# Kernel optimization log

Hardware: AMD Instinct MI355X
Metric: run time of the kernel (lower is better)

## Reference

```python
import jax, jax.numpy as jnp
import numpy as np

N_NODES = 100000
N_EDGES = 1600000
D_IN = 256
D_OUT = 64
AVG_DEG = N_EDGES // N_NODES  # 16


def setup_inputs() -> dict:
    key = jax.random.key(0)
    k1, k2, k3 = jax.random.split(key, 3)
    X = jax.random.normal(k1, (N_NODES, D_IN), dtype=jnp.float32)
    weights = jax.random.normal(k2, (D_IN, D_OUT), dtype=jnp.float32) * (1.0 / np.sqrt(D_IN))
    # CSR with uniform degree for a valid structure (load balance is a kernel concern, not math)
    row_pointers = jnp.arange(N_NODES + 1, dtype=jnp.int64) * AVG_DEG
    column_index = jax.random.randint(k3, (N_EDGES,), 0, N_NODES, dtype=jnp.int64)
    # GNNAdvisor precomputes degrees as d^{-1/2} for symmetric GCN normalization
    deg = (row_pointers[1:] - row_pointers[:-1]).astype(jnp.float32)
    degrees = 1.0 / jnp.sqrt(jnp.maximum(deg, 1.0))
    return {"X": X, "weights": weights, "row_pointers": row_pointers,
            "column_index": column_index, "degrees": degrees}


def reference(X, weights, row_pointers, column_index, degrees):
    # Dense transform: [N, D_in] @ [D_in, D_out] -> [N, D_out]
    X_prime = jnp.matmul(X, weights)
    E = column_index.shape[0]
    # CSR row ids for each edge (destination node of the aggregation)
    row_ids = jnp.searchsorted(row_pointers, jnp.arange(E, dtype=row_pointers.dtype), side='right') - 1
    # out[i] = d_i^{-1/2} * sum_{j in N(i)} d_j^{-1/2} * X'[j]
    gathered = X_prime[column_index] * degrees[column_index][:, None]  # [E, D_out]
    agg = jax.ops.segment_sum(gathered, row_ids, num_segments=row_pointers.shape[0] - 1)
    return agg * degrees[:, None]
```

## Files before the change

### kernel.cpp

```cpp
#include <hip/hip_runtime.h>
#include <hip/hip_bf16.h>


constexpr int D_IN  = 256;
constexpr int D_OUT = 64;
constexpr int WT_LD = D_IN + 8;

typedef short  s8v  __attribute__((ext_vector_type(8)));
typedef __bf16 bf8v __attribute__((ext_vector_type(8)));
typedef float  f32x4 __attribute__((ext_vector_type(4)));
typedef unsigned short us8v __attribute__((ext_vector_type(8)));

union BF8 { bf8v b; s8v s; };

__global__ __launch_bounds__(256) void gemm_bf16_kernel(
    const float* __restrict__ X, const float* __restrict__ W,
    const float* __restrict__ deg, unsigned short* __restrict__ Xp, int n)
{
    __shared__ __bf16 Wt[D_OUT][WT_LD];

    const int tid = threadIdx.x;

    #pragma unroll
    for (int i = 0; i < 16; ++i) {
        const int f4 = tid + i * 256;
        const int k  = f4 >> 4;
        const int c4 = (f4 & 15) * 4;
        const float4 w = *reinterpret_cast<const float4*>(&W[(size_t)k * D_OUT + c4]);
        Wt[c4 + 0][k] = (__bf16)w.x;
        Wt[c4 + 1][k] = (__bf16)w.y;
        Wt[c4 + 2][k] = (__bf16)w.z;
        Wt[c4 + 3][k] = (__bf16)w.w;
    }
    __syncthreads();

    const int wid  = tid >> 6;
    const int lane = tid & 63;
    const int lrow = lane & 15;
    const int kgrp = lane >> 4;

    const int row0 = blockIdx.x * 64 + wid * 16;
    if (row0 >= n) return;
    const int grow = row0 + lrow;
    const int xr   = grow < n ? grow : n - 1;

    f32x4 acc[4] = {};

    const float* xrow = X + (size_t)xr * D_IN + kgrp * 8;
    const __bf16* wt0 = &Wt[lrow][kgrp * 8];

    #pragma unroll
    for (int ks = 0; ks < 8; ++ks) {
        const int k0 = ks * 32;
        const float4 x0 = *reinterpret_cast<const float4*>(xrow + k0);
        const float4 x1 = *reinterpret_cast<const float4*>(xrow + k0 + 4);
        BF8 xf;
        xf.b[0] = (__bf16)x0.x; xf.b[1] = (__bf16)x0.y;
        xf.b[2] = (__bf16)x0.z; xf.b[3] = (__bf16)x0.w;
        xf.b[4] = (__bf16)x1.x; xf.b[5] = (__bf16)x1.y;
        xf.b[6] = (__bf16)x1.z; xf.b[7] = (__bf16)x1.w;

        #pragma unroll
        for (int f = 0; f < 4; ++f) {
            const s8v wf = *reinterpret_cast<const s8v*>(wt0 + (size_t)f * 16 * WT_LD + k0);
            acc[f] = __builtin_amdgcn_mfma_f32_16x16x32_bf16(wf, xf.s, acc[f], 0, 0, 0);
        }
    }

    if (grow < n) {
        const float d = deg[grow];
        #pragma unroll
        for (int f = 0; f < 4; ++f) {
            ushort4 v;
            __bf16 b0 = (__bf16)(acc[f][0] * d);
            __bf16 b1 = (__bf16)(acc[f][1] * d);
            __bf16 b2 = (__bf16)(acc[f][2] * d);
            __bf16 b3 = (__bf16)(acc[f][3] * d);
            v.x = *reinterpret_cast<unsigned short*>(&b0);
            v.y = *reinterpret_cast<unsigned short*>(&b1);
            v.z = *reinterpret_cast<unsigned short*>(&b2);
            v.w = *reinterpret_cast<unsigned short*>(&b3);
            *reinterpret_cast<ushort4*>(
                &Xp[(size_t)grow * D_OUT + f * 16 + kgrp * 4]) = v;
        }
    }
}

__global__ __launch_bounds__(256) void agg_kernel(
    const unsigned short* __restrict__ Xp, const int* __restrict__ rp,
    const int* __restrict__ ci, const float* __restrict__ deg,
    float* __restrict__ out, int n)
{
    const int node = blockIdx.x * 32 + (threadIdx.x >> 3);
    if (node >= n) return;
    const int c8 = (threadIdx.x & 7) * 8;

    const int e0 = rp[node];
    const int e1 = rp[node + 1];

    float acc[8] = {};
    int e = e0;
    for (; e + 4 <= e1; e += 4) {
        const int j0 = ci[e + 0];
        const int j1 = ci[e + 1];
        const int j2 = ci[e + 2];
        const int j3 = ci[e + 3];
        const us8v v0 = *reinterpret_cast<const us8v*>(&Xp[(size_t)j0 * D_OUT + c8]);
        const us8v v1 = *reinterpret_cast<const us8v*>(&Xp[(size_t)j1 * D_OUT + c8]);
        const us8v v2 = *reinterpret_cast<const us8v*>(&Xp[(size_t)j2 * D_OUT + c8]);
        const us8v v3 = *reinterpret_cast<const us8v*>(&Xp[(size_t)j3 * D_OUT + c8]);
        #pragma unroll
        for (int j = 0; j < 8; ++j) {
            acc[j] += __uint_as_float((unsigned)v0[j] << 16);
            acc[j] += __uint_as_float((unsigned)v1[j] << 16);
            acc[j] += __uint_as_float((unsigned)v2[j] << 16);
            acc[j] += __uint_as_float((unsigned)v3[j] << 16);
        }
    }
    for (; e < e1; ++e) {
        const us8v v = *reinterpret_cast<const us8v*>(&Xp[(size_t)ci[e] * D_OUT + c8]);
        #pragma unroll
        for (int j = 0; j < 8; ++j)
            acc[j] += __uint_as_float((unsigned)v[j] << 16);
    }

    const float d = deg[node];
    float4 o0 = make_float4(acc[0] * d, acc[1] * d, acc[2] * d, acc[3] * d);
    float4 o1 = make_float4(acc[4] * d, acc[5] * d, acc[6] * d, acc[7] * d);
    float* op = out + (size_t)node * D_OUT + c8;
    *reinterpret_cast<float4*>(op)     = o0;
    *reinterpret_cast<float4*>(op + 4) = o1;
}

extern "C" void kernel_launch(void* const* d_in, const int* in_sizes, int n_in,
                              void* d_out, int out_size, void* d_ws, size_t ws_size,
                              hipStream_t stream)
{
    const float* X   = (const float*)d_in[0];
    const float* W   = (const float*)d_in[1];
    const int*   rp  = (const int*)d_in[2];
    const int*   ci  = (const int*)d_in[3];
    const float* deg = (const float*)d_in[4];
    float* out = (float*)d_out;
    unsigned short* Xp = (unsigned short*)d_ws;

    const int n = in_sizes[4];

    const int gemm_blocks = (n + 63) / 64;
    gemm_bf16_kernel<<<gemm_blocks, 256, 0, stream>>>(X, W, deg, Xp, n);

    const int agg_blocks = (n + 31) / 32;
    agg_kernel<<<agg_blocks, 256, 0, stream>>>(Xp, rp, ci, deg, out, n);
}
```

Measured before the change: 57.32 us.

## Pre-transpose weights once, make GEMM persistent, batch 16 gathers in aggregation

Adds a tiny kernel that converts and transposes W to bf16 in workspace once, so each GEMM block copies it into shared memory with vector loads instead of redoing the scattered transpose. The GEMM becomes a grid-stride persistent kernel with 391 blocks that loop over 16-row tiles, which amortises the weight staging across many tiles. The aggregation adds a fast path for degree-16 aligned rows that loads the indices as int4 and issues all 16 neighbour gathers before accumulating, raising memory-level parallelism at the cost of more registers. It also adds an extra kernel launch, and the fixed grid size may leave some compute units underused.

```diff
diff --git a/kernel.cpp b/kernel.cpp
--- a/kernel.cpp
+++ b/kernel.cpp
@@ -13,24 +13,30 @@
 
 union BF8 { bf8v b; s8v s; };
 
+__global__ void prep_w_kernel(const float* __restrict__ W,
+                              unsigned short* __restrict__ Wt_g)
+{
+    const int c = blockIdx.x;
+    const int k = threadIdx.x;
+    __bf16 b = (__bf16)W[(size_t)k * D_OUT + c];
+    Wt_g[(size_t)c * D_IN + k] = *reinterpret_cast<unsigned short*>(&b);
+}
+
 __global__ __launch_bounds__(256) void gemm_bf16_kernel(
-    const float* __restrict__ X, const float* __restrict__ W,
-    const float* __restrict__ deg, unsigned short* __restrict__ Xp, int n)
+    const float* __restrict__ X, const unsigned short* __restrict__ Wt_g,
+    const float* __restrict__ deg, unsigned short* __restrict__ Xp,
+    int n, int ntiles)
 {
-    __shared__ __bf16 Wt[D_OUT][WT_LD];
+    __shared__ unsigned short Wt[D_OUT][WT_LD];
 
     const int tid = threadIdx.x;
 
-    #pragma unroll
-    for (int i = 0; i < 16; ++i) {
-        const int f4 = tid + i * 256;
-        const int k  = f4 >> 4;
-        const int c4 = (f4 & 15) * 4;
-        const float4 w = *reinterpret_cast<const float4*>(&W[(size_t)k * D_OUT + c4]);
-        Wt[c4 + 0][k] = (__bf16)w.x;
-        Wt[c4 + 1][k] = (__bf16)w.y;
-        Wt[c4 + 2][k] = (__bf16)w.z;
-        Wt[c4 + 3][k] = (__bf16)w.w;
+    {
+        const int c = tid >> 2, seg = tid & 3;
+        const us8v* src = reinterpret_cast<const us8v*>(Wt_g + (size_t)c * D_IN + seg * 64);
+        us8v* dst = reinterpret_cast<us8v*>(&Wt[c][seg * 64]);
+        #pragma unroll
+        for (int i = 0; i < 8; ++i) dst[i] = src[i];
     }
     __syncthreads();
 
@@ -39,49 +45,50 @@
     const int lrow = lane & 15;
     const int kgrp = lane >> 4;
 
-    const int row0 = blockIdx.x * 64 + wid * 16;
-    if (row0 >= n) return;
-    const int grow = row0 + lrow;
-    const int xr   = grow < n ? grow : n - 1;
+    const unsigned short* wt0 = &Wt[lrow][kgrp * 8];
+    const int wstride = gridDim.x << 2;
 
-    f32x4 acc[4] = {};
+    for (int tile = blockIdx.x * 4 + wid; tile < ntiles; tile += wstride) {
+        const int grow = tile * 16 + lrow;
+        const int xr   = grow < n ? grow : n - 1;
+        const float* xrow = X + (size_t)xr * D_IN + kgrp * 8;
 
-    const float* xrow = X + (size_t)xr * D_IN + kgrp * 8;
-    const __bf16* wt0 = &Wt[lrow][kgrp * 8];
-
-    #pragma unroll
-    for (int ks = 0; ks < 8; ++ks) {
-        const int k0 = ks * 32;
-        const float4 x0 = *reinterpret_cast<const float4*>(xrow + k0);
-        const float4 x1 = *reinterpret_cast<const float4*>(xrow + k0 + 4);
-        BF8 xf;
-        xf.b[0] = (__bf16)x0.x; xf.b[1] = (__bf16)x0.y;
-        xf.b[2] = (__bf16)x0.z; xf.b[3] = (__bf16)x0.w;
-        xf.b[4] = (__bf16)x1.x; xf.b[5] = (__bf16)x1.y;
-        xf.b[6] = (__bf16)x1.z; xf.b[7] = (__bf16)x1.w;
+        f32x4 acc[4] = {};
 
         #pragma unroll
-        for (int f = 0; f < 4; ++f) {
-            const s8v wf = *reinterpret_cast<const s8v*>(wt0 + (size_t)f * 16 * WT_LD + k0);
-            acc[f] = __builtin_amdgcn_mfma_f32_16x16x32_bf16(wf, xf.s, acc[f], 0, 0, 0);
+        for (int ks = 0; ks < 8; ++ks) {
+            const float4 x0 = *reinterpret_cast<const float4*>(xrow + ks * 32);
+            const float4 x1 = *reinterpret_cast<const float4*>(xrow + ks * 32 + 4);
+            BF8 xf;
+            xf.b[0] = (__bf16)x0.x; xf.b[1] = (__bf16)x0.y;
+            xf.b[2] = (__bf16)x0.z; xf.b[3] = (__bf16)x0.w;
+            xf.b[4] = (__bf16)x1.x; xf.b[5] = (__bf16)x1.y;
+            xf.b[6] = (__bf16)x1.z; xf.b[7] = (__bf16)x1.w;
+
+            #pragma unroll
+            for (int f = 0; f < 4; ++f) {
+                const s8v wf = *reinterpret_cast<const s8v*>(
+                    wt0 + (size_t)f * 16 * WT_LD + ks * 32);
+                acc[f] = __builtin_amdgcn_mfma_f32_16x16x32_bf16(wf, xf.s, acc[f], 0, 0, 0);
+            }
         }
-    }
 
-    if (grow < n) {
-        const float d = deg[grow];
-        #pragma unroll
-        for (int f = 0; f < 4; ++f) {
-            ushort4 v;
-            __bf16 b0 = (__bf16)(acc[f][0] * d);
-            __bf16 b1 = (__bf16)(acc[f][1] * d);
-            __bf16 b2 = (__bf16)(acc[f][2] * d);
-            __bf16 b3 = (__bf16)(acc[f][3] * d);
-            v.x = *reinterpret_cast<unsigned short*>(&b0);
-            v.y = *reinterpret_cast<unsigned short*>(&b1);
-            v.z = *reinterpret_cast<unsigned short*>(&b2);
-            v.w = *reinterpret_cast<unsigned short*>(&b3);
-            *reinterpret_cast<ushort4*>(
-                &Xp[(size_t)grow * D_OUT + f * 16 + kgrp * 4]) = v;
+        if (grow < n) {
+            const float d = deg[grow];
+            #pragma unroll
+            for (int f = 0; f < 4; ++f) {
+                ushort4 v;
+                __bf16 b0 = (__bf16)(acc[f][0] * d);
+                __bf16 b1 = (__bf16)(acc[f][1] * d);
+                __bf16 b2 = (__bf16)(acc[f][2] * d);
+                __bf16 b3 = (__bf16)(acc[f][3] * d);
+                v.x = *reinterpret_cast<unsigned short*>(&b0);
+                v.y = *reinterpret_cast<unsigned short*>(&b1);
+                v.z = *reinterpret_cast<unsigned short*>(&b2);
+                v.w = *reinterpret_cast<unsigned short*>(&b3);
+                *reinterpret_cast<ushort4*>(
+                    &Xp[(size_t)grow * D_OUT + f * 16 + kgrp * 4]) = v;
+            }
         }
     }
 }
@@ -97,39 +104,42 @@
 
     const int e0 = rp[node];
     const int e1 = rp[node + 1];
+    const int m  = e1 - e0;
 
     float acc[8] = {};
-    int e = e0;
-    for (; e + 4 <= e1; e += 4) {
-        const int j0 = ci[e + 0];
-        const int j1 = ci[e + 1];
-        const int j2 = ci[e + 2];
-        const int j3 = ci[e + 3];
-        const us8v v0 = *reinterpret_cast<const us8v*>(&Xp[(size_t)j0 * D_OUT + c8]);
-        const us8v v1 = *reinterpret_cast<const us8v*>(&Xp[(size_t)j1 * D_OUT + c8]);
-        const us8v v2 = *reinterpret_cast<const us8v*>(&Xp[(size_t)j2 * D_OUT + c8]);
-        const us8v v3 = *reinterpret_cast<const us8v*>(&Xp[(size_t)j3 * D_OUT + c8]);
+
+    if (m == 16 && (e0 & 3) == 0) {
+        int4 i4[4];
         #pragma unroll
-        for (int j = 0; j < 8; ++j) {
-            acc[j] += __uint_as_float((unsigned)v0[j] << 16);
-            acc[j] += __uint_as_float((unsigned)v1[j] << 16);
-            acc[j] += __uint_as_float((unsigned)v2[j] << 16);
-            acc[j] += __uint_as_float((unsigned)v3[j] << 16);
+        for (int b = 0; b < 4; ++b)
+            i4[b] = *reinterpret_cast<const int4*>(&ci[e0 + b * 4]);
+        const int idx[16] = { i4[0].x, i4[0].y, i4[0].z, i4[0].w,
+                              i4[1].x, i4[1].y, i4[1].z, i4[1].w,
+                              i4[2].x, i4[2].y, i4[2].z, i4[2].w,
+                              i4[3].x, i4[3].y, i4[3].z, i4[3].w };
+        us8v v[16];
+        #pragma unroll
+        for (int j = 0; j < 16; ++j)
+            v[j] = *reinterpret_cast<const us8v*>(&Xp[(size_t)idx[j] * D_OUT + c8]);
+        #pragma unroll
+        for (int j = 0; j < 16; ++j) {
+            #pragma unroll
+            for (int k = 0; k < 8; ++k)
+                acc[k] += __uint_as_float((unsigned)v[j][k] << 16);
         }
-    }
-    for (; e < e1; ++e) {
-        const us8v v = *reinterpret_cast<const us8v*>(&Xp[(size_t)ci[e] * D_OUT + c8]);
-        #pragma unroll
-        for (int j = 0; j < 8; ++j)
-            acc[j] += __uint_as_float((unsigned)v[j] << 16);
+    } else {
+        for (int e = e0; e < e1; ++e) {
+            const us8v v = *reinterpret_cast<const us8v*>(&Xp[(size_t)ci[e] * D_OUT + c8]);
+            #pragma unroll
+            for (int k = 0; k < 8; ++k)
+                acc[k] += __uint_as_float((unsigned)v[k] << 16);
+        }
     }
 
     const float d = deg[node];
-    float4 o0 = make_float4(acc[0] * d, acc[1] * d, acc[2] * d, acc[3] * d);
-    float4 o1 = make_float4(acc[4] * d, acc[5] * d, acc[6] * d, acc[7] * d);
     float* op = out + (size_t)node * D_OUT + c8;
-    *reinterpret_cast<float4*>(op)     = o0;
-    *reinterpret_cast<float4*>(op + 4) = o1;
+    *reinterpret_cast<float4*>(op)     = make_float4(acc[0]*d, acc[1]*d, acc[2]*d, acc[3]*d);
+    *reinterpret_cast<float4*>(op + 4) = make_float4(acc[4]*d, acc[5]*d, acc[6]*d, acc[7]*d);
 }
 
 extern "C" void kernel_launch(void* const* d_in, const int* in_sizes, int n_in,
@@ -142,12 +152,16 @@
     const int*   ci  = (const int*)d_in[3];
     const float* deg = (const float*)d_in[4];
     float* out = (float*)d_out;
-    unsigned short* Xp = (unsigned short*)d_ws;
 
     const int n = in_sizes[4];
 
-    const int gemm_blocks = (n + 63) / 64;
-    gemm_bf16_kernel<<<gemm_blocks, 256, 0, stream>>>(X, W, deg, Xp, n);
+    unsigned short* Xp   = (unsigned short*)d_ws;
+    unsigned short* Wt_g = (unsigned short*)((char*)d_ws + (16u << 20));
+
+    prep_w_kernel<<<D_OUT, D_IN, 0, stream>>>(W, Wt_g);
+
+    const int ntiles = (n + 15) / 16;
+    gemm_bf16_kernel<<<391, 256, 0, stream>>>(X, Wt_g, deg, Xp, n, ntiles);
 
     const int agg_blocks = (n + 31) / 32;
     agg_kernel<<<agg_blocks, 256, 0, stream>>>(Xp, rp, ci, deg, out, n);
```

After: 60.36 us. +5.3%, slower.
